# Performance work log

Measured on AMD Instinct MI355X. Metric: run time of the kernel, lower is better.

The kernel has to match this reference:

```python
import jax, jax.numpy as jnp
import numpy as np
from jax import lax

B, IN_C, OUT_C, K, Z_DIM, H, W = 32, 128, 128, 3, 64, 96, 96
PAD = K // 2


def setup_inputs() -> dict:
    key = jax.random.key(0)
    k1, k2, k3, k4, k5, k6 = jax.random.split(key, 6)
    fan = (2.0 / (IN_C * K * K)) ** 0.5
    x = jax.random.normal(k1, (B, IN_C, H, W), dtype=jnp.float32)
    z = jax.random.normal(k2, (B, Z_DIM), dtype=jnp.float32)
    base_weight = jax.random.normal(k3, (OUT_C, IN_C, K, K), dtype=jnp.float32) * fan
    # torch nn.Linear weights are [out_features, in_features]
    gate_weight = jax.random.normal(k4, (OUT_C, Z_DIM), dtype=jnp.float32) * (1.0 / Z_DIM ** 0.5)
    pw_weight = jax.random.normal(k5, (OUT_C * IN_C, Z_DIM), dtype=jnp.float32) * (1.0 / Z_DIM ** 0.5)
    dw_weight = jax.random.normal(k6, (OUT_C * K * K, Z_DIM), dtype=jnp.float32) * (1.0 / Z_DIM ** 0.5)
    return {"x": x, "z": z, "base_weight": base_weight, "gate_weight": gate_weight,
            "pw_weight": pw_weight, "dw_weight": dw_weight}


def _merged_weight(z, base_weight, gate_weight, pw_weight, dw_weight):
    # BaseOp.get_weight: base * gate(z)  -> [B, out_c, in_c, k, k]
    gate = z @ gate_weight.T                       # [B, out_c]
    w_base = base_weight[None] * gate[:, :, None, None, None]
    # PWOp.get_weight (groups=1): [B, out_c, in_c, 1, 1]
    pw = (z @ pw_weight.T).reshape(B, OUT_C, IN_C)
    # DWOp.get_weight: [B, out_c, 1, k, k]
    dw = (z @ dw_weight.T).reshape(B, OUT_C, 1, K, K)
    # delta = pw * dw broadcast -> [B, out_c, in_c, k, k]
    delta = pw[:, :, :, None, None] * dw
    return w_base + delta


def _per_sample_conv(xi, wi):
    # xi: [in_c, H, W], wi: [out_c, in_c, k, k]
    return lax.conv_general_dilated(
        xi[None], wi, window_strides=(1, 1),
        padding=((PAD, PAD), (PAD, PAD)),
        dimension_numbers=("NCHW", "OIHW", "NCHW"))[0]


def reference(x, z, base_weight, gate_weight, pw_weight, dw_weight):
    w = _merged_weight(z, base_weight, gate_weight, pw_weight, dw_weight)
    return jax.vmap(_per_sample_conv)(x, w)  # [B, out_c, H, W]
```

## Files before the change

kernel.cpp:

```cpp
#include <hip/hip_runtime.h>
#include <hip/hip_bf16.h>

typedef __bf16 bf16x8 __attribute__((ext_vector_type(8)));
typedef float f32x4 __attribute__((ext_vector_type(4)));
typedef float f32x16 __attribute__((ext_vector_type(16)));

__device__ __forceinline__ void load_lds16(const void* g, void* l) {
  __builtin_amdgcn_global_load_lds((const __attribute__((address_space(1))) void*)g,
                                   (__attribute__((address_space(3))) void*)l, 16, 0, 0);
}

__global__ __launch_bounds__(512) void prep_x_kernel(const float* __restrict__ x,
                                                     __hip_bfloat16* __restrict__ xn) {
  __shared__ float tile[128][97];
  int h = blockIdx.x;
  int b = blockIdx.y;
  const float* src = x + (size_t)b * 128 * 9216 + h * 96;
  for (int f = threadIdx.x; f < 3072; f += 512) {
    int ic = f / 24, w4 = f - ic * 24;
    float4 v = *(const float4*)(src + (size_t)ic * 9216 + w4 * 4);
    tile[ic][w4 * 4 + 0] = v.x; tile[ic][w4 * 4 + 1] = v.y;
    tile[ic][w4 * 4 + 2] = v.z; tile[ic][w4 * 4 + 3] = v.w;
  }
  __syncthreads();
  __hip_bfloat16* bb  = xn + (size_t)b * 4 * 307328;
  __hip_bfloat16* dst = bb + (h + 1) * 3136 + 32;
  for (int o = threadIdx.x; o < 1536; o += 512) {
    int grp = o / 384, rem = o - grp * 384;
    int w = rem >> 2, chunk = rem & 3;
    __hip_bfloat16 tmp[8];
    #pragma unroll
    for (int e = 0; e < 8; e++) tmp[e] = __float2bfloat16(tile[grp * 32 + chunk * 8 + e][w]);
    *(uint4*)(dst + (size_t)grp * 307328 + w * 32 + chunk * 8) = *(uint4*)tmp;
  }
  if (threadIdx.x < 32) {
    int u = threadIdx.x;
    int grp = u >> 3, rem = u & 7;
    int pw = (rem >> 2) ? 97 : 0, k = rem & 3;
    *(uint4*)(bb + (size_t)grp * 307328 + ((h + 1) * 98 + pw) * 32 + k * 8) = make_uint4(0, 0, 0, 0);
  }
  if (h == 0 || h == 95) {
    int ph = (h == 0) ? 0 : 97;
    for (int u = threadIdx.x; u < 1568; u += 512) {
      int grp = u / 392, rem = u - grp * 392;
      int pw = rem >> 2, k = rem & 3;
      *(uint4*)(bb + (size_t)grp * 307328 + (ph * 98 + pw) * 32 + k * 8) = make_uint4(0, 0, 0, 0);
    }
  }
}

__global__ __launch_bounds__(256) void prep_w_kernel(
    const float* __restrict__ z, const float* __restrict__ gw,
    const float* __restrict__ pww, const float* __restrict__ dww,
    const float* __restrict__ base, __hip_bfloat16* __restrict__ Wt) {
  __shared__ float zs[256];
  __shared__ float res[138][5];
  int oc = blockIdx.x & 127;
  int b0 = (blockIdx.x >> 7) * 4;
  zs[threadIdx.x] = z[b0 * 64 + threadIdx.x];
  __syncthreads();
  int row = threadIdx.x;
  if (row < 138) {
    const float* wrow = (row == 0) ? gw + (size_t)oc * 64
                      : (row < 10) ? dww + ((size_t)oc * 9 + (row - 1)) * 64
                                   : pww + ((size_t)oc * 128 + (row - 10)) * 64;
    float wr[64];
    #pragma unroll
    for (int i = 0; i < 16; i++) {
      float4 v = ((const float4*)wrow)[i];
      wr[4*i] = v.x; wr[4*i+1] = v.y; wr[4*i+2] = v.z; wr[4*i+3] = v.w;
    }
    #pragma unroll
    for (int bb = 0; bb < 4; bb++) {
      float a = 0.f;
      #pragma unroll
      for (int i = 0; i < 64; i++) a += zs[bb * 64 + i] * wr[i];
      res[row][bb] = a;
    }
  }
  __syncthreads();
  for (int e = threadIdx.x; e < 2304; e += 256) {
    int icp = e & 15;
    int r1 = e >> 4;
    int tap = r1 % 9, gb = r1 / 9;
    int grp = gb & 3, bb = gb >> 2;
    int b = b0 + bb;
    int ic = grp * 32 + icp * 2;
    int dy = tap / 3, dx = tap - dy * 3;
    float g = res[0][bb], d = res[1 + tap][bb];
    float p0 = res[10 + ic][bb], p1 = res[11 + ic][bb];
    const float* bp = base + ((size_t)(oc * 128 + ic)) * 9 + tap;
    __hip_bfloat162 o2 = {__float2bfloat16(bp[0] * g + p0 * d),
                          __float2bfloat16(bp[9] * g + p1 * d)};
    *(__hip_bfloat162*)(Wt + ((((size_t)(b * 4 + grp)) * 9 + dx * 3 + dy) * 128 + oc) * 32 + icp * 2) = o2;
  }
}

__global__ __launch_bounds__(256, 3) void conv_kernel(
    const __hip_bfloat16* __restrict__ xn, const __hip_bfloat16* __restrict__ Wt,
    float* __restrict__ out) {
  __shared__ __align__(16) char smem[49152];

  int bid = blockIdx.x;
  int X = bid & 7, q = bid >> 3;
  int logical = X * 288 + q;
  int b   = logical / 72;
  int rem = logical - b * 72;
  int ocg = rem & 1;
  int t36 = rem >> 1;
  int hr  = t36 / 3;
  int wc  = t36 - hr * 3;
  int h0 = hr * 8, w0 = wc * 32;

  int tid = threadIdx.x;
  int lane = tid & 63, wid = tid >> 6;
  int l31 = lane & 31, lh = lane >> 5;
  int wm = wid >> 1, wn = wid & 1;

  char* const xr0 = smem;
  char* const xr1 = smem + 24576;
  const char* xp0 = xr0 + wm * 4 * 2176 + l31 * 16 + lh * 544;
  const char* xp1 = xr1 + wm * 4 * 2176 + l31 * 16 + lh * 544;

  int xoff[6];
  #pragma unroll
  for (int j = 0; j < 6; j++) {
    int t = j * 256 + tid; if (t > 1359) t = 1359;
    int hh = t / 136, r2 = t - hh * 136;
    int k = r2 / 34, ww = r2 - k * 34;
    xoff[j] = ((h0 + hh) * 98 + (w0 + ww)) * 32 + k * 8;
  }

  const __hip_bfloat16* xbase = xn + (size_t)b * 4 * 307328;
  const __hip_bfloat16* wlb =
      Wt + (size_t)b * 147456 + (ocg * 64 + wn * 32 + l31) * 32 + lh * 8;

  f32x16 acc[4];
  #pragma unroll
  for (int i = 0; i < 4; i++)
    #pragma unroll
    for (int e = 0; e < 16; e++) acc[i][e] = 0.f;

  bf16x8 wreg[3][2];

  #pragma unroll
  for (int j = 0; j < 6; j++)
    load_lds16(xbase + xoff[j], xr0 + ((j * 256 + wid * 64) << 4));
  #pragma unroll
  for (int dy = 0; dy < 3; dy++)
    #pragma unroll
    for (int kk = 0; kk < 2; kk++)
      wreg[dy][kk] = *(const bf16x8*)(wlb + dy * 4096 + kk * 16);

#define PH(S)                                                                      \
  {                                                                                \
    constexpr int grp_ = (S) / 3, dx_ = (S) % 3;                                   \
        \
    if constexpr (dx_ == 0 && grp_ < 3) {                                          \
      char* xd_ = (((grp_ + 1) & 1) ? xr1 : xr0);                                  \
      const __hip_bfloat16* xsrc = xbase + (size_t)(grp_ + 1) * 307328;            \
      _Pragma("unroll")                                                            \
      for (int j = 0; j < 6; j++)                                                  \
        load_lds16(xsrc + xoff[j], xd_ + ((j * 256 + wid * 64) << 4));             \
    }                                                                              \
    if constexpr ((S) == 0) {                                                      \
      asm volatile("s_waitcnt vmcnt(12)" ::: "memory");                            \
      __builtin_amdgcn_s_barrier();                                                \
    }                                                                              \
    const char* xw_ = ((grp_ & 1) ? xp1 : xp0);                                    \
    bf16x8 afr[6][2];                                                              \
    _Pragma("unroll")                                                              \
    for (int rr = 0; rr < 6; rr++)                                                 \
      _Pragma("unroll")                                                            \
      for (int kk = 0; kk < 2; kk++)                                               \
        afr[rr][kk] = *(const bf16x8*)(xw_ + rr * 2176 + kk * 1088 + dx_ * 16);    \
    _Pragma("unroll")                                                              \
    for (int dy = 0; dy < 3; dy++) {                                               \
      __builtin_amdgcn_s_setprio(1);                                               \
      _Pragma("unroll")                                                            \
      for (int kk = 0; kk < 2; kk++)                                               \
        _Pragma("unroll")                                                          \
        for (int i = 0; i < 4; i++)                                                \
          acc[i] = __builtin_amdgcn_mfma_f32_32x32x16_bf16(afr[i + dy][kk],        \
                        wreg[dy][kk], acc[i], 0, 0, 0);                            \
      __builtin_amdgcn_s_setprio(0);                                               \
      if constexpr ((S) < 11) {                                                    \
        constexpr int sn_ = (S) + 1;                                               \
        constexpr int g2_ = sn_ / 3, dxn_ = sn_ % 3;                               \
        _Pragma("unroll")                                                          \
        for (int kk = 0; kk < 2; kk++)                                             \
          wreg[dy][kk] = *(const bf16x8*)(wlb + g2_ * 36864 +                      \
              (dxn_ * 3 + dy) * 4096 + kk * 16);                                   \
      }                                                                            \
    }                                                                              \
        \
         \
    if constexpr (dx_ == 2 && grp_ < 3) {                                          \
      __builtin_amdgcn_s_barrier();                                                \
    }                                                                              \
  }

  PH(0)  PH(1)  PH(2)
  PH(3)  PH(4)  PH(5)
  PH(6)  PH(7)  PH(8)
  PH(9)  PH(10) PH(11)
#undef PH

  #pragma unroll
  for (int i = 0; i < 4; i++) {
    int h = h0 + wm * 4 + i;
    int oc = ocg * 64 + wn * 32 + l31;
    float* op = out + ((size_t)b * 128 + oc) * 9216 + h * 96 + w0 + 4 * lh;
    #pragma unroll
    for (int qq = 0; qq < 4; qq++) {
      f32x4 v = {acc[i][4 * qq + 0], acc[i][4 * qq + 1],
                 acc[i][4 * qq + 2], acc[i][4 * qq + 3]};
      *(f32x4*)(op + 8 * qq) = v;
    }
  }
}

extern "C" void kernel_launch(void* const* d_in, const int* in_sizes, int n_in,
                              void* d_out, int out_size, void* d_ws, size_t ws_size,
                              hipStream_t stream) {
  const float* x   = (const float*)d_in[0];
  const float* z   = (const float*)d_in[1];
  const float* bw  = (const float*)d_in[2];
  const float* gw  = (const float*)d_in[3];
  const float* pww = (const float*)d_in[4];
  const float* dww = (const float*)d_in[5];
  float* out = (float*)d_out;

  char* ws = (char*)d_ws;
  __hip_bfloat16* xn = (__hip_bfloat16*)ws;
  __hip_bfloat16* Wt = (__hip_bfloat16*)(ws + 78675968);

  hipLaunchKernelGGL(prep_x_kernel, dim3(96, 32), dim3(512), 0, stream, x, xn);
  hipLaunchKernelGGL(prep_w_kernel, dim3(1024), dim3(256), 0, stream,
                     z, gw, pww, dww, bw, Wt);
  hipLaunchKernelGGL(conv_kernel,   dim3(2304), dim3(256), 0, stream, xn, Wt, out);
}
```

Baseline: 152.8 us.

## Remap warp tile to 2 rows by 64 output channels per wave

Each wave now computes 2 output rows for all 64 channels of the group, instead of 4 rows for 32 channels. Per phase it reads 4 row fragments from LDS rather than 6, reducing LDS read traffic and row-halo overlap, and reuses each A fragment across two weight fragments. The cost is a larger weight register set (12 bf16x8 vectors) loaded redundantly by every wave from global memory. The k-loop is reordered so weight prefetch happens after the second k-slice, which shortens the load latency window and raises register pressure.

Result: slower. 168.8 us (+10.5%).

```diff
diff --git a/kernel.cpp b/kernel.cpp
--- a/kernel.cpp
+++ b/kernel.cpp
@@ -115,12 +115,11 @@
   int tid = threadIdx.x;
   int lane = tid & 63, wid = tid >> 6;
   int l31 = lane & 31, lh = lane >> 5;
-  int wm = wid >> 1, wn = wid & 1;
 
   char* const xr0 = smem;
   char* const xr1 = smem + 24576;
-  const char* xp0 = xr0 + wm * 4 * 2176 + l31 * 16 + lh * 544;
-  const char* xp1 = xr1 + wm * 4 * 2176 + l31 * 16 + lh * 544;
+  const char* xp0 = xr0 + wid * 2 * 2176 + l31 * 16 + lh * 544;
+  const char* xp1 = xr1 + wid * 2 * 2176 + l31 * 16 + lh * 544;
 
   int xoff[6];
   #pragma unroll
@@ -133,15 +132,17 @@
 
   const __hip_bfloat16* xbase = xn + (size_t)b * 4 * 307328;
   const __hip_bfloat16* wlb =
-      Wt + (size_t)b * 147456 + (ocg * 64 + wn * 32 + l31) * 32 + lh * 8;
-
-  f32x16 acc[4];
-  #pragma unroll
-  for (int i = 0; i < 4; i++)
-    #pragma unroll
-    for (int e = 0; e < 16; e++) acc[i][e] = 0.f;
-
-  bf16x8 wreg[3][2];
+      Wt + (size_t)b * 147456 + (ocg * 64 + l31) * 32 + lh * 8;
+
+  f32x16 acc[2][2];
+  #pragma unroll
+  for (int i = 0; i < 2; i++)
+    #pragma unroll
+    for (int n = 0; n < 2; n++)
+      #pragma unroll
+      for (int e = 0; e < 16; e++) acc[i][n][e] = 0.f;
+
+  bf16x8 wreg[3][2][2];
 
   #pragma unroll
   for (int j = 0; j < 6; j++)
@@ -149,8 +150,10 @@
   #pragma unroll
   for (int dy = 0; dy < 3; dy++)
     #pragma unroll
-    for (int kk = 0; kk < 2; kk++)
-      wreg[dy][kk] = *(const bf16x8*)(wlb + dy * 4096 + kk * 16);
+    for (int n = 0; n < 2; n++)
+      #pragma unroll
+      for (int kk = 0; kk < 2; kk++)
+        wreg[dy][n][kk] = *(const bf16x8*)(wlb + dy * 4096 + n * 1024 + kk * 16);
 
 #define PH(S)                                                                      \
   {                                                                                \
@@ -168,33 +171,36 @@
       __builtin_amdgcn_s_barrier();                                                \
     }                                                                              \
     const char* xw_ = ((grp_ & 1) ? xp1 : xp0);                                    \
-    bf16x8 afr[6][2];                                                              \
     _Pragma("unroll")                                                              \
-    for (int rr = 0; rr < 6; rr++)                                                 \
+    for (int kk = 0; kk < 2; kk++) {                                               \
+      bf16x8 afr[4];                                                               \
       _Pragma("unroll")                                                            \
-      for (int kk = 0; kk < 2; kk++)                                               \
-        afr[rr][kk] = *(const bf16x8*)(xw_ + rr * 2176 + kk * 1088 + dx_ * 16);    \
-    _Pragma("unroll")                                                              \
-    for (int dy = 0; dy < 3; dy++) {                                               \
+      for (int rr = 0; rr < 4; rr++)                                               \
+        afr[rr] = *(const bf16x8*)(xw_ + rr * 2176 + kk * 1088 + dx_ * 16);        \
       __builtin_amdgcn_s_setprio(1);                                               \
       _Pragma("unroll")                                                            \
-      for (int kk = 0; kk < 2; kk++)                                               \
+      for (int dy = 0; dy < 3; dy++) {                                             \
         _Pragma("unroll")                                                          \
-        for (int i = 0; i < 4; i++)                                                \
-          acc[i] = __builtin_amdgcn_mfma_f32_32x32x16_bf16(afr[i + dy][kk],        \
-                        wreg[dy][kk], acc[i], 0, 0, 0);                            \
+        for (int i = 0; i < 2; i++)                                                \
+          _Pragma("unroll")                                                        \
+          for (int n = 0; n < 2; n++)                                              \
+            acc[i][n] = __builtin_amdgcn_mfma_f32_32x32x16_bf16(afr[i + dy],       \
+                            wreg[dy][n][kk], acc[i][n], 0, 0, 0);                  \
+              \
+        if (kk == 1 && (S) < 11) {                                                 \
+          constexpr int sn_ = (S) + 1;                                             \
+          constexpr int g2_ = sn_ / 3, dxn_ = sn_ % 3;                             \
+          _Pragma("unroll")                                                        \
+          for (int n = 0; n < 2; n++)                                              \
+            _Pragma("unroll")                                                      \
+            for (int k2 = 0; k2 < 2; k2++)                                         \
+              wreg[dy][n][k2] = *(const bf16x8*)(wlb + g2_ * 36864 +               \
+                  (dxn_ * 3 + dy) * 4096 + n * 1024 + k2 * 16);                    \
+        }                                                                          \
+      }                                                                            \
       __builtin_amdgcn_s_setprio(0);                                               \
-      if constexpr ((S) < 11) {                                                    \
-        constexpr int sn_ = (S) + 1;                                               \
-        constexpr int g2_ = sn_ / 3, dxn_ = sn_ % 3;                               \
-        _Pragma("unroll")                                                          \
-        for (int kk = 0; kk < 2; kk++)                                             \
-          wreg[dy][kk] = *(const bf16x8*)(wlb + g2_ * 36864 +                      \
-              (dxn_ * 3 + dy) * 4096 + kk * 16);                                   \
-      }                                                                            \
-    }                                                                              \
-        \
-         \
+    }                                                                              \
+                        \
     if constexpr (dx_ == 2 && grp_ < 3) {                                          \
       __builtin_amdgcn_s_barrier();                                                \
     }                                                                              \
@@ -207,15 +213,18 @@
 #undef PH
 
   #pragma unroll
-  for (int i = 0; i < 4; i++) {
-    int h = h0 + wm * 4 + i;
-    int oc = ocg * 64 + wn * 32 + l31;
-    float* op = out + ((size_t)b * 128 + oc) * 9216 + h * 96 + w0 + 4 * lh;
-    #pragma unroll
-    for (int qq = 0; qq < 4; qq++) {
-      f32x4 v = {acc[i][4 * qq + 0], acc[i][4 * qq + 1],
-                 acc[i][4 * qq + 2], acc[i][4 * qq + 3]};
-      *(f32x4*)(op + 8 * qq) = v;
+  for (int i = 0; i < 2; i++) {
+    int h = h0 + wid * 2 + i;
+    #pragma unroll
+    for (int n = 0; n < 2; n++) {
+      int oc = ocg * 64 + n * 32 + l31;
+      float* op = out + ((size_t)b * 128 + oc) * 9216 + h * 96 + w0 + 4 * lh;
+      #pragma unroll
+      for (int qq = 0; qq < 4; qq++) {
+        f32x4 v = {acc[i][n][4 * qq + 0], acc[i][n][4 * qq + 1],
+                   acc[i][n][4 * qq + 2], acc[i][n][4 * qq + 3]};
+        *(f32x4*)(op + 8 * qq) = v;
+      }
     }
   }
 }
```
